# Performance work log

Measured on AMD Instinct MI355X. Metric: run time of the kernel, lower is better.

The kernel has to match this reference:

```python
import jax, jax.numpy as jnp
import numpy as np

N_GRAPHS = 32
N_NODES = 2048          # nodes per graph == lstm1 input_size
N_TOTAL = N_GRAPHS * N_NODES
N_EDGES = 1048576
HEADS = 8
GAT_OUT = 12            # per-head GAT output dim (== num_features)
OUT_CH = 9
NEG_SLOPE = 0.2
BN_EPS = 1e-5


def setup_inputs() -> dict:
    key = jax.random.key(0)
    ks = jax.random.split(key, 20)
    inp = {}
    inp['x'] = jax.random.normal(ks[0], (N_TOTAL, GAT_OUT), jnp.float32)
    inp['edge_index'] = jax.random.randint(ks[1], (2, N_EDGES), 0, N_TOTAL, jnp.int64)
    inp['W_gat'] = jax.random.normal(ks[2], (GAT_OUT, HEADS * GAT_OUT), jnp.float32) * 0.3
    inp['a_src'] = jax.random.normal(ks[3], (HEADS, GAT_OUT), jnp.float32) * 0.3
    inp['a_dst'] = jax.random.normal(ks[4], (HEADS, GAT_OUT), jnp.float32) * 0.3
    inp['gat_bias'] = jax.random.normal(ks[5], (GAT_OUT,), jnp.float32) * 0.1
    inp['bn_gamma'] = jax.random.uniform(ks[6], (GAT_OUT,), jnp.float32, 0.5, 1.5)
    inp['bn_beta'] = jax.random.normal(ks[7], (GAT_OUT,), jnp.float32) * 0.1
    inp['bn_mean'] = jax.random.normal(ks[8], (GAT_OUT,), jnp.float32) * 0.1
    inp['bn_var'] = jax.random.uniform(ks[9], (GAT_OUT,), jnp.float32, 0.5, 1.5)
    inp['w_ih1'] = jax.random.normal(ks[10], (4 * 32, N_NODES), jnp.float32) / np.sqrt(N_NODES)
    inp['w_hh1'] = jax.random.normal(ks[11], (4 * 32, 32), jnp.float32) / np.sqrt(32)
    inp['b_ih1'] = jnp.zeros((4 * 32,), jnp.float32)
    inp['b_hh1'] = jnp.zeros((4 * 32,), jnp.float32)
    inp['w_ih2'] = jax.random.normal(ks[12], (4 * 128, 32), jnp.float32) / np.sqrt(32)
    inp['w_hh2'] = jax.random.normal(ks[13], (4 * 128, 128), jnp.float32) / np.sqrt(128)
    inp['b_ih2'] = jnp.zeros((4 * 128,), jnp.float32)
    inp['b_hh2'] = jnp.zeros((4 * 128,), jnp.float32)
    inp['lin_w'] = jax.random.normal(ks[14], (N_NODES, 128), jnp.float32) / np.sqrt(128)
    inp['lin_b'] = jax.random.normal(ks[15], (N_NODES,), jnp.float32) * 0.1
    return inp


def _gat(x, edge_index, W, a_src, a_dst, bias):
    # PyG GATConv, heads=HEADS, out=GAT_OUT, concat=False (mean over heads), eval mode.
    N = x.shape[0]
    xp = (x @ W).reshape(N, HEADS, GAT_OUT)               # [N,H,C]
    loops = jnp.arange(N, dtype=edge_index.dtype)
    src = jnp.concatenate([edge_index[0], loops])
    dst = jnp.concatenate([edge_index[1], loops])
    asrc = jnp.einsum('nhc,hc->nh', xp, a_src)            # [N,H]
    adst = jnp.einsum('nhc,hc->nh', xp, a_dst)
    e = jax.nn.leaky_relu(asrc[src] + adst[dst], NEG_SLOPE)  # [E,H]
    m = jax.ops.segment_max(e, dst, num_segments=N)
    e = jnp.exp(e - m[dst])
    denom = jax.ops.segment_sum(e, dst, num_segments=N)
    alpha = e / (denom[dst] + 1e-16)
    msg = xp[src] * alpha[:, :, None]                     # [E,H,C]
    out = jax.ops.segment_sum(msg, dst, num_segments=N)   # [N,H,C]
    return out.mean(axis=1) + bias                        # concat=False -> head mean


def _lstm(x_seq, w_ih, w_hh, b_ih, b_hh):
    # x_seq: [T,B,I]; PyTorch gate order i,f,g,o.
    Hh = w_hh.shape[1]
    B = x_seq.shape[1]
    bias = b_ih + b_hh

    def step(carry, xt):
        h, c = carry
        gates = xt @ w_ih.T + h @ w_hh.T + bias
        i, f, g, o = jnp.split(gates, 4, axis=-1)
        c = jax.nn.sigmoid(f) * c + jax.nn.sigmoid(i) * jnp.tanh(g)
        h = jax.nn.sigmoid(o) * jnp.tanh(c)
        return (h, c), h

    init = (jnp.zeros((B, Hh), x_seq.dtype), jnp.zeros((B, Hh), x_seq.dtype))
    _, hs = jax.lax.scan(step, init, x_seq)
    return hs


def reference(x, edge_index, W_gat, a_src, a_dst, gat_bias,
              bn_gamma, bn_beta, bn_mean, bn_var,
              w_ih1, w_hh1, b_ih1, b_hh1,
              w_ih2, w_hh2, b_ih2, b_hh2,
              lin_w, lin_b):
    h = _gat(x, edge_index, W_gat, a_src, a_dst, gat_bias)          # [N,12]
    h = (h - bn_mean) / jnp.sqrt(bn_var + BN_EPS) * bn_gamma + bn_beta
    # dropout inactive in eval mode
    h = jax.nn.log_softmax(h, axis=1)
    h = h.reshape(N_GRAPHS, N_NODES, GAT_OUT)
    h = jnp.moveaxis(h, 2, 0)                                       # [T=12,B,n]
    h = _lstm(h, w_ih1, w_hh1, b_ih1, b_hh1)                        # [12,B,32]
    h = _lstm(h, w_ih2, w_hh2, b_ih2, b_hh2)                        # [12,B,128]
    h = h @ lin_w.T + lin_b                                         # [12,B,n]
    h = h[-OUT_CH:]                                                 # [9,B,n]
    h = jnp.moveaxis(h, 0, 2)                                       # [B,n,9]
    return h.reshape(N_GRAPHS * N_NODES, OUT_CH)
```

## Files before the change

kernel.cpp:

```cpp
#include <hip/hip_runtime.h>
#include <math.h>

#define N_EDGES_C 1048576
#define N_TOTAL_C 65536

typedef _Float16 h2v __attribute__((ext_vector_type(2)));
typedef int i4v __attribute__((ext_vector_type(4)));

#if defined(__has_builtin)
#if __has_builtin(__builtin_amdgcn_fdot2)
#define HAS_FDOT2 1
#endif
#if __has_builtin(__builtin_amdgcn_rcpf)
#define HAS_RCPF 1
#endif
#endif

__device__ __forceinline__ float fdot2(h2v a, h2v b, float c) {
#ifdef HAS_FDOT2
    return __builtin_amdgcn_fdot2(a, b, c, false);
#else
    return c + (float)a.x * (float)b.x + (float)a.y * (float)b.y;
#endif
}

__device__ __forceinline__ float fast_rcp(float x) {
#ifdef HAS_RCPF
    return __builtin_amdgcn_rcpf(x);
#else
    return 1.0f / x;
#endif
}
__device__ __forceinline__ float sigf(float x){ return fast_rcp(1.0f + __expf(-x)); }
__device__ __forceinline__ float tanh_fast(float x){ return fmaf(2.0f, fast_rcp(1.0f + __expf(-2.0f*x)), -1.0f); }
__device__ __forceinline__ float lrelu(float x){ return (x>=0.f)? x : 0.2f*x; }


__global__ void prep_kernel(const float* __restrict__ x, const float* __restrict__ Wg,
                            const float* __restrict__ a_src, const float* __restrict__ a_dst,
                            _Float16* __restrict__ xpp)
{
    int tid = threadIdx.x;
    __shared__ float Ws[12*96];
    __shared__ float as_s[96], ad_s[96];
    for (int i = tid; i < 1152; i += 256) Ws[i] = Wg[i];
    if (tid < 96) { as_s[tid] = a_src[tid]; ad_s[tid] = a_dst[tid]; }
    __syncthreads();
    int gid = blockIdx.x * 256 + tid;
    int n = gid >> 3;
    int h = gid & 7;
    const float4* xv = (const float4*)(x + (size_t)n * 12);
    float4 v0 = xv[0], v1 = xv[1], v2 = xv[2];
    float xr[12] = {v0.x,v0.y,v0.z,v0.w, v1.x,v1.y,v1.z,v1.w, v2.x,v2.y,v2.z,v2.w};
    float xp_[12];
    #pragma unroll
    for (int c = 0; c < 12; c++) {
        float acc = 0.f;
        #pragma unroll
        for (int k = 0; k < 12; k++) acc += xr[k] * Ws[k*96 + h*12 + c];
        xp_[c] = acc;
    }
    float sa = 0.f, sd = 0.f;
    #pragma unroll
    for (int c = 0; c < 12; c++) { sa += xp_[c]*as_s[h*12+c]; sd += xp_[c]*ad_s[h*12+c]; }
    union { _Float16 hh[16]; float ff[8]; float4 f4[2]; } s;
    #pragma unroll
    for (int c = 0; c < 12; c++) s.hh[c] = (_Float16)xp_[c];
    s.ff[6] = sa;
    s.ff[7] = sd;
    float4* o = (float4*)(xpp + (size_t)gid * 16);
    o[0] = s.f4[0];
    o[1] = s.f4[1];
}

__global__ __launch_bounds__(256)
void edge_hist(const int* __restrict__ ei, unsigned* __restrict__ cnt,
               unsigned* __restrict__ rank8)
{
    __shared__ unsigned hist[16384];
    int tid = threadIdx.x;
    int slice = blockIdx.x;
    for (int i = tid; i < 16384; i += 256) hist[i] = 0;
    __syncthreads();
    const i4v* dst4 = (const i4v*)(ei + N_EDGES_C) + slice*2048;
    for (int i = tid; i < 2048; i += 256) {
        i4v d = __builtin_nontemporal_load(&dst4[i]);
        int dd[4] = {d.x, d.y, d.z, d.w};
        unsigned packed = 0;
        #pragma unroll
        for (int j = 0; j < 4; j++) {
            int dj = dd[j];
            unsigned sh = (unsigned)(dj & 3) << 3;
            unsigned old = atomicAdd(&hist[dj >> 2], 1u << sh);
            packed |= ((old >> sh) & 0xffu) << (j*8);
        }
        __builtin_nontemporal_store(packed, &rank8[slice*2048 + i]);
    }
    __syncthreads();
    unsigned* cg = cnt + (size_t)slice*16384;
    for (int i = tid; i < 16384; i += 256) cg[i] = hist[i];
}

__global__ void slice_prefix(unsigned* __restrict__ cnt, int* __restrict__ deg)
{
    int w = blockIdx.x*128 + threadIdx.x;
    unsigned run = 0;
    unsigned* base = cnt + w;
    for (int s = 0; s < 128; s++) {
        unsigned v = base[(size_t)s*16384];
        base[(size_t)s*16384] = run;
        run += v;
    }
    ((int4*)deg)[w] = make_int4((int)(run & 255u), (int)((run >> 8) & 255u),
                                (int)((run >> 16) & 255u), (int)(run >> 24));
}

__global__ void scan_build(const int* __restrict__ deg, int* __restrict__ rowptr)
{
    __shared__ int sums[1024];
    int tid = threadIdx.x;
    int4 v[16];
    const int4* deg4 = (const int4*)deg;
    #pragma unroll
    for (int j = 0; j < 16; j++) v[j] = deg4[tid*16 + j];
    int s = 0;
    #pragma unroll
    for (int j = 0; j < 16; j++) s += v[j].x + v[j].y + v[j].z + v[j].w;
    sums[tid] = s;
    __syncthreads();
    for (int off = 1; off < 1024; off <<= 1) {
        int t = 0;
        if (tid >= off) t = sums[tid - off];
        __syncthreads();
        if (tid >= off) sums[tid] += t;
        __syncthreads();
    }
    int run = sums[tid] - s;
    int4* rp4 = (int4*)rowptr;
    #pragma unroll
    for (int j = 0; j < 16; j++) {
        int4 r;
        r.x = run; run += v[j].x;
        r.y = run; run += v[j].y;
        r.z = run; run += v[j].z;
        r.w = run; run += v[j].w;
        rp4[tid*16 + j] = r;
    }
    if (tid == 1023) rowptr[65536] = run;
}

__global__ __launch_bounds__(256)
void edge_scatter(const int* __restrict__ ei, const unsigned* __restrict__ rank8,
                  const unsigned* __restrict__ cnt, const int* __restrict__ rowptr,
                  int* __restrict__ csr)
{
    __shared__ unsigned pos_s[2048];
    __shared__ int src_s[2048];
    int slice = blockIdx.x >> 2;
    int quar  = blockIdx.x & 3;
    int base = slice*2048 + quar*512;
    const i4v* dst4 = (const i4v*)(ei + N_EDGES_C);
    const i4v* src4 = (const i4v*)ei;
    const unsigned* cslice = cnt + (size_t)slice*16384;
    for (int i = threadIdx.x; i < 512; i += 256) {
        int idx = base + i;
        i4v d = __builtin_nontemporal_load(&dst4[idx]);
        i4v s = __builtin_nontemporal_load(&src4[idx]);
        unsigned r = __builtin_nontemporal_load(&rank8[idx]);
        int dd[4] = {d.x, d.y, d.z, d.w};
        int ss[4] = {s.x, s.y, s.z, s.w};
        #pragma unroll
        for (int j = 0; j < 4; j++) {
            int dj = dd[j];
            unsigned word = cslice[dj >> 2];
            int so = (int)((word >> ((unsigned)(dj & 3) << 3)) & 0xffu);
            int rk = (int)((r >> (j*8)) & 0xffu);
            unsigned pos = (unsigned)(rowptr[dj] + so + rk);
            pos_s[i*4 + j] = pos | ((unsigned)(dj >> 13) << 24);
            src_s[i*4 + j] = ss[j];
        }
    }
    __syncthreads();
    #pragma unroll 1
    for (unsigned g = 0; g < 8; g++) {
        for (int e = threadIdx.x; e < 2048; e += 256) {
            unsigned pw = pos_s[e];
            if ((pw >> 24) == g) csr[pw & 0xFFFFFFu] = src_s[e];
        }
    }
}

__global__ void gat_aggregate(const _Float16* __restrict__ xpp,
                              const int* __restrict__ rowptr, const int* __restrict__ csr_src,
                              const float* __restrict__ gat_bias, const float* __restrict__ bn_gamma,
                              const float* __restrict__ bn_beta, const float* __restrict__ bn_mean,
                              const float* __restrict__ bn_var, float* __restrict__ seq)
{
    int gid = blockIdx.x * 256 + threadIdx.x;
    int n = gid >> 3;
    int h = gid & 7;

    float acc[12];
    float adst_n, d;
    {
        const float4* p = (const float4*)(xpp + (size_t)n*128 + h*16);
        float4 f0 = p[0], f1 = p[1];
        adst_n = f1.w;
        float w = __expf(lrelu(f1.z + adst_n));
        d = w;
        h2v c0 = __builtin_bit_cast(h2v, f0.x), c1 = __builtin_bit_cast(h2v, f0.y);
        h2v c2 = __builtin_bit_cast(h2v, f0.z), c3 = __builtin_bit_cast(h2v, f0.w);
        h2v c4 = __builtin_bit_cast(h2v, f1.x), c5 = __builtin_bit_cast(h2v, f1.y);
        acc[0]=w*(float)c0.x; acc[1]=w*(float)c0.y; acc[2]=w*(float)c1.x; acc[3]=w*(float)c1.y;
        acc[4]=w*(float)c2.x; acc[5]=w*(float)c2.y; acc[6]=w*(float)c3.x; acc[7]=w*(float)c3.y;
        acc[8]=w*(float)c4.x; acc[9]=w*(float)c4.y; acc[10]=w*(float)c5.x; acc[11]=w*(float)c5.y;
    }

    auto accum = [&](float4 f0, float4 f1) {
        float w = __expf(lrelu(f1.z + adst_n));
        d += w;
        h2v c0 = __builtin_bit_cast(h2v, f0.x), c1 = __builtin_bit_cast(h2v, f0.y);
        h2v c2 = __builtin_bit_cast(h2v, f0.z), c3 = __builtin_bit_cast(h2v, f0.w);
        h2v c4 = __builtin_bit_cast(h2v, f1.x), c5 = __builtin_bit_cast(h2v, f1.y);
        acc[0]+=w*(float)c0.x; acc[1]+=w*(float)c0.y; acc[2]+=w*(float)c1.x; acc[3]+=w*(float)c1.y;
        acc[4]+=w*(float)c2.x; acc[5]+=w*(float)c2.y; acc[6]+=w*(float)c3.x; acc[7]+=w*(float)c3.y;
        acc[8]+=w*(float)c4.x; acc[9]+=w*(float)c4.y; acc[10]+=w*(float)c5.x; acc[11]+=w*(float)c5.y;
    };

    int beg = rowptr[n], end = rowptr[n+1];
    const _Float16* xh = xpp + (size_t)h * 16;
    int i = beg;
    for (; i + 4 <= end; i += 4) {
        int s0 = csr_src[i+0];
        int s1 = csr_src[i+1];
        int s2 = csr_src[i+2];
        int s3 = csr_src[i+3];
        const float4* p0 = (const float4*)(xh + (size_t)s0*128);
        const float4* p1 = (const float4*)(xh + (size_t)s1*128);
        const float4* p2 = (const float4*)(xh + (size_t)s2*128);
        const float4* p3 = (const float4*)(xh + (size_t)s3*128);
        float4 a0 = p0[0], b0 = p0[1];
        float4 a1 = p1[0], b1 = p1[1];
        float4 a2 = p2[0], b2 = p2[1];
        float4 a3 = p3[0], b3 = p3[1];
        accum(a0, b0);
        accum(a1, b1);
        accum(a2, b2);
        accum(a3, b3);
    }
    for (; i < end; i++) {
        int src = csr_src[i];
        const float4* p = (const float4*)(xh + (size_t)src*128);
        float4 f0 = p[0], f1 = p[1];
        accum(f0, f1);
    }

    float inv = 1.0f / (d + 1e-16f);
    float res[12];
    #pragma unroll
    for (int c = 0; c < 12; c++) {
        float v = acc[c] * inv;
        v += __shfl_xor(v, 1);
        v += __shfl_xor(v, 2);
        v += __shfl_xor(v, 4);
        res[c] = v * 0.125f;
    }
    if (h == 0) {
        float vals[12];
        float mx = -1e30f;
        #pragma unroll
        for (int c = 0; c < 12; c++) {
            float v = res[c] + gat_bias[c];
            v = (v - bn_mean[c]) * rsqrtf(bn_var[c] + 1e-5f) * bn_gamma[c] + bn_beta[c];
            vals[c] = v;
            mx = fmaxf(mx, v);
        }
        float sum = 0.f;
        #pragma unroll
        for (int c = 0; c < 12; c++) sum += __expf(vals[c] - mx);
        float lse = __logf(sum) + mx;
        #pragma unroll
        for (int c = 0; c < 12; c++) seq[(size_t)c * N_TOTAL_C + n] = vals[c] - lse;
    }
}

__global__ void gemm_x1(const float* __restrict__ A, const float* __restrict__ B,
                        float* __restrict__ C)
{
    __shared__ float As[32][33], Bs[32][33];
    const int K = 2048, N = 128;
    int tid = threadIdx.x;
    int tx = tid & 31, ty = tid >> 5;
    int bm = blockIdx.x * 32, bn = blockIdx.y * 32;
    int kbase = blockIdx.z * 128;
    float acc[4] = {0.f,0.f,0.f,0.f};
    for (int kk = 0; kk < 128; kk += 32) {
        int k0 = kbase + kk;
        #pragma unroll
        for (int i = 0; i < 4; i++) {
            int r = ty + i*8;
            As[r][tx] = A[(size_t)(bm + r) * K + k0 + tx];
            Bs[r][tx] = B[(size_t)(bn + r) * K + k0 + tx];
        }
        __syncthreads();
        #pragma unroll
        for (int k = 0; k < 32; k++) {
            float bv = Bs[tx][k];
            #pragma unroll
            for (int i = 0; i < 4; i++) acc[i] += As[ty + i*8][k] * bv;
        }
        __syncthreads();
    }
    #pragma unroll
    for (int i = 0; i < 4; i++)
        atomicAdd(&C[(size_t)(bm + ty + i*8) * N + bn + tx], acc[i]);
}

__global__ __launch_bounds__(512)
void lstm_fused(const float* __restrict__ X1, const float* __restrict__ w_hh1,
                const float* __restrict__ b_ih1, const float* __restrict__ b_hh1,
                const float* __restrict__ w_ih2, const float* __restrict__ w_hh2,
                const float* __restrict__ b_ih2, const float* __restrict__ b_hh2,
                float* __restrict__ H2)
{
    __shared__ float whh1[128*33];
    __shared__ float b1s[128];
    __shared__ float h1[32], c1[32];
    __shared__ __align__(16) _Float16 h1s[32];
    __shared__ __align__(16) _Float16 h2s[128];
    __shared__ float c2[128];
    __shared__ float g1s[128], g2s[512];
    int tid = threadIdx.x;
    int b = blockIdx.x;

    h2v whh[64];
    {
        const float2* wh = (const float2*)(w_hh2 + (size_t)tid * 128);
        #pragma unroll
        for (int k = 0; k < 64; k++) {
            float2 v = wh[k];
            h2v t; t.x = (_Float16)v.x; t.y = (_Float16)v.y;
            whh[k] = t;
        }
    }
    h2v wih[16];
    {
        const float2* wi = (const float2*)(w_ih2 + (size_t)tid * 32);
        #pragma unroll
        for (int k = 0; k < 16; k++) {
            float2 v = wi[k];
            h2v t; t.x = (_Float16)v.x; t.y = (_Float16)v.y;
            wih[k] = t;
        }
    }
    float b2 = b_ih2[tid] + b_hh2[tid];

    for (int i = tid; i < 128*32; i += 512) whh1[(i >> 5)*33 + (i & 31)] = w_hh1[i];
    if (tid < 128) b1s[tid] = b_ih1[tid] + b_hh1[tid];
    if (tid < 32)  { h1[tid] = 0.f; c1[tid] = 0.f; h1s[tid] = (_Float16)0.f; }
    if (tid < 128) { c2[tid] = 0.f; h2s[tid] = (_Float16)0.f; }

    float xv = 0.f;
    if (tid < 128) xv = X1[((size_t)0*32 + b)*128 + tid];
    __syncthreads();

    for (int t = 0; t < 12; t++) {
        float xv_next = 0.f;
        if (t < 11 && tid < 128) xv_next = X1[((size_t)(t+1)*32 + b)*128 + tid];

        float p0 = b2, p1 = 0.f, p2 = 0.f, p3 = 0.f;
        #pragma unroll
        for (int j = 0; j < 16; j++) {
            float4 f = ((const float4*)h2s)[j];
            p0 = fdot2(__builtin_bit_cast(h2v, f.x), whh[j*4+0], p0);
            p1 = fdot2(__builtin_bit_cast(h2v, f.y), whh[j*4+1], p1);
            p2 = fdot2(__builtin_bit_cast(h2v, f.z), whh[j*4+2], p2);
            p3 = fdot2(__builtin_bit_cast(h2v, f.w), whh[j*4+3], p3);
        }
        float acc2 = (p0 + p1) + (p2 + p3);

        if (tid < 128) {
            const float* wr = &whh1[tid * 33];
            float acc = xv + b1s[tid];
            #pragma unroll
            for (int k = 0; k < 32; k++) acc += h1[k] * wr[k];
            g1s[tid] = acc;
        }
        __syncthreads();
        if (tid < 32) {
            float ig = sigf(g1s[tid]), fg = sigf(g1s[32+tid]);
            float gg = tanh_fast(g1s[64+tid]), og = sigf(g1s[96+tid]);
            float cn = fg * c1[tid] + ig * gg;
            c1[tid] = cn;
            float hn = og * tanh_fast(cn);
            h1[tid] = hn;
            h1s[tid] = (_Float16)hn;
        }
        __syncthreads();
        {
            float q0 = 0.f, q1 = 0.f, q2 = 0.f, q3 = 0.f;
            #pragma unroll
            for (int j = 0; j < 4; j++) {
                float4 f = ((const float4*)h1s)[j];
                q0 = fdot2(__builtin_bit_cast(h2v, f.x), wih[j*4+0], q0);
                q1 = fdot2(__builtin_bit_cast(h2v, f.y), wih[j*4+1], q1);
                q2 = fdot2(__builtin_bit_cast(h2v, f.z), wih[j*4+2], q2);
                q3 = fdot2(__builtin_bit_cast(h2v, f.w), wih[j*4+3], q3);
            }
            g2s[tid] = acc2 + (q0 + q1) + (q2 + q3);
        }
        __syncthreads();
        if (tid < 128) {
            float ig = sigf(g2s[tid]), fg = sigf(g2s[128+tid]);
            float gg = tanh_fast(g2s[256+tid]), og = sigf(g2s[384+tid]);
            float cn = fg * c2[tid] + ig * gg;
            c2[tid] = cn;
            float hn = og * tanh_fast(cn);
            h2s[tid] = (_Float16)hn;
            if (t >= 3) H2[((size_t)t*32 + b)*128 + tid] = hn;
        }
        __syncthreads();
        xv = xv_next;
    }
}

__global__ void gemm_out(const float* __restrict__ A, const float* __restrict__ B,
                         const float* __restrict__ bias, float* __restrict__ out)
{
    __shared__ float As[32][33], Bs[32][33];
    const int K = 128;
    int tid = threadIdx.x;
    int tx = tid & 31, ty = tid >> 5;
    int bm = blockIdx.x * 32, bn = blockIdx.y * 32;
    float acc[4] = {0.f,0.f,0.f,0.f};
    for (int k0 = 0; k0 < K; k0 += 32) {
        #pragma unroll
        for (int i = 0; i < 4; i++) {
            int r = ty + i*8;
            As[r][tx] = A[(size_t)(bm + r) * K + k0 + tx];
            Bs[r][tx] = B[(size_t)(bn + r) * K + k0 + tx];
        }
        __syncthreads();
        #pragma unroll
        for (int kk = 0; kk < 32; kk++) {
            float bv = Bs[tx][kk];
            #pragma unroll
            for (int i = 0; i < 4; i++) acc[i] += As[ty + i*8][kk] * bv;
        }
        __syncthreads();
    }
    int j = blockIdx.x;
    int nn = bn + tx;
    float bv = bias[nn];
    #pragma unroll
    for (int i = 0; i < 4; i++) {
        int bb = ty + i*8;
        out[((size_t)bb * 2048 + nn) * 9 + j] = acc[i] + bv;
    }
}

extern "C" void kernel_launch(void* const* d_in, const int* in_sizes, int n_in,
                              void* d_out, int out_size, void* d_ws, size_t ws_size,
                              hipStream_t stream)
{
    const float* x        = (const float*)d_in[0];
    const int*   ei       = (const int*)  d_in[1];
    const float* W_gat    = (const float*)d_in[2];
    const float* a_src    = (const float*)d_in[3];
    const float* a_dst    = (const float*)d_in[4];
    const float* gat_bias = (const float*)d_in[5];
    const float* bn_gamma = (const float*)d_in[6];
    const float* bn_beta  = (const float*)d_in[7];
    const float* bn_mean  = (const float*)d_in[8];
    const float* bn_var   = (const float*)d_in[9];
    const float* w_ih1    = (const float*)d_in[10];
    const float* w_hh1    = (const float*)d_in[11];
    const float* b_ih1    = (const float*)d_in[12];
    const float* b_hh1    = (const float*)d_in[13];
    const float* w_ih2    = (const float*)d_in[14];
    const float* w_hh2    = (const float*)d_in[15];
    const float* b_ih2    = (const float*)d_in[16];
    const float* b_hh2    = (const float*)d_in[17];
    const float* lin_w    = (const float*)d_in[18];
    const float* lin_b    = (const float*)d_in[19];
    float* out = (float*)d_out;

    float* ws = (float*)d_ws;
    _Float16* xpp = (_Float16*)ws;
    float* seq  = ws + 4194304;
    float* X1   = seq + 786432;
    float* H2   = X1  + 49152;
    int* rowptr = (int*)(H2 + 49152);
    int* deg    = rowptr + 65544;
    unsigned* cnt = (unsigned*)(deg + 65536);
    unsigned* rank8 = cnt + 2097152;
    int* csr    = (int*)(rank8 + 262144);

    hipMemsetAsync(X1, 0, 49152 * sizeof(float), stream);
    prep_kernel <<<2048, 256, 0, stream>>>(x, W_gat, a_src, a_dst, xpp);
    edge_hist   <<<128, 256, 0, stream>>>(ei, cnt, rank8);
    slice_prefix<<<128, 128, 0, stream>>>(cnt, deg);
    scan_build  <<<1, 1024, 0, stream>>>(deg, rowptr);
    edge_scatter<<<512, 256, 0, stream>>>(ei, rank8, cnt, rowptr, csr);
    gat_aggregate<<<2048, 256, 0, stream>>>(xpp, rowptr, csr,
                                            gat_bias, bn_gamma, bn_beta, bn_mean, bn_var, seq);
    gemm_x1<<<dim3(12, 4, 16), 256, 0, stream>>>(seq, w_ih1, X1);
    lstm_fused<<<32, 512, 0, stream>>>(X1, w_hh1, b_ih1, b_hh1, w_ih2, w_hh2, b_ih2, b_hh2, H2);
    gemm_out<<<dim3(9, 64), 256, 0, stream>>>(H2 + 96*128, lin_w, lin_b, out);
}
```

Before: 254.5 us.

## Store projected features head-major and split GAT aggregation per head with reduce kernel

The projected node features are now stored head-major (one contiguous 65536-node plane per head), and the aggregation kernel assigns a whole block to a single head, so each per-edge gather reads 32 bytes from a 2 MB per-head plane instead of a strided slice of a node-major array. The intent is better cache locality for the random source gathers. Per-head results go to a partial buffer, and a new reduce kernel averages the heads and applies bias, batch norm and log-softmax, which costs an extra launch and extra global traffic. The slice_prefix loop is also batched into 32 loads before the stores to raise memory-level parallelism.

```diff
diff --git a/kernel.cpp b/kernel.cpp
--- a/kernel.cpp
+++ b/kernel.cpp
@@ -46,9 +46,8 @@
     for (int i = tid; i < 1152; i += 256) Ws[i] = Wg[i];
     if (tid < 96) { as_s[tid] = a_src[tid]; ad_s[tid] = a_dst[tid]; }
     __syncthreads();
-    int gid = blockIdx.x * 256 + tid;
-    int n = gid >> 3;
-    int h = gid & 7;
+    int h = tid >> 5;
+    int n = blockIdx.x * 32 + (tid & 31);
     const float4* xv = (const float4*)(x + (size_t)n * 12);
     float4 v0 = xv[0], v1 = xv[1], v2 = xv[2];
     float xr[12] = {v0.x,v0.y,v0.z,v0.w, v1.x,v1.y,v1.z,v1.w, v2.x,v2.y,v2.z,v2.w};
@@ -68,7 +67,7 @@
     for (int c = 0; c < 12; c++) s.hh[c] = (_Float16)xp_[c];
     s.ff[6] = sa;
     s.ff[7] = sd;
-    float4* o = (float4*)(xpp + (size_t)gid * 16);
+    float4* o = (float4*)(xpp + ((size_t)h * 65536 + n) * 16);
     o[0] = s.f4[0];
     o[1] = s.f4[1];
 }
@@ -101,15 +100,22 @@
     for (int i = tid; i < 16384; i += 256) cg[i] = hist[i];
 }
 
-__global__ void slice_prefix(unsigned* __restrict__ cnt, int* __restrict__ deg)
+__global__ __launch_bounds__(128)
+void slice_prefix(unsigned* __restrict__ cnt, int* __restrict__ deg)
 {
     int w = blockIdx.x*128 + threadIdx.x;
     unsigned run = 0;
     unsigned* base = cnt + w;
-    for (int s = 0; s < 128; s++) {
-        unsigned v = base[(size_t)s*16384];
-        base[(size_t)s*16384] = run;
-        run += v;
+    #pragma unroll 1
+    for (int s = 0; s < 128; s += 32) {
+        unsigned v[32];
+        #pragma unroll
+        for (int k = 0; k < 32; k++) v[k] = base[(size_t)(s+k)*16384];
+        #pragma unroll
+        for (int k = 0; k < 32; k++) {
+            base[(size_t)(s+k)*16384] = run;
+            run += v[k];
+        }
     }
     ((int4*)deg)[w] = make_int4((int)(run & 255u), (int)((run >> 8) & 255u),
                                 (int)((run >> 16) & 255u), (int)(run >> 24));
@@ -190,20 +196,19 @@
     }
 }
 
-__global__ void gat_aggregate(const _Float16* __restrict__ xpp,
-                              const int* __restrict__ rowptr, const int* __restrict__ csr_src,
-                              const float* __restrict__ gat_bias, const float* __restrict__ bn_gamma,
-                              const float* __restrict__ bn_beta, const float* __restrict__ bn_mean,
-                              const float* __restrict__ bn_var, float* __restrict__ seq)
-{
-    int gid = blockIdx.x * 256 + threadIdx.x;
-    int n = gid >> 3;
-    int h = gid & 7;
+__global__ __launch_bounds__(256)
+void gat_aggregate(const _Float16* __restrict__ xpp,
+                   const int* __restrict__ rowptr, const int* __restrict__ csr_src,
+                   float* __restrict__ partial)
+{
+    int head = blockIdx.x & 7;
+    int n = (blockIdx.x >> 3) * 256 + threadIdx.x;
+    const _Float16* xh = xpp + (size_t)head * (65536 * 16);
 
     float acc[12];
     float adst_n, d;
     {
-        const float4* p = (const float4*)(xpp + (size_t)n*128 + h*16);
+        const float4* p = (const float4*)(xh + (size_t)n * 16);
         float4 f0 = p[0], f1 = p[1];
         adst_n = f1.w;
         float w = __expf(lrelu(f1.z + adst_n));
@@ -228,17 +233,16 @@
     };
 
     int beg = rowptr[n], end = rowptr[n+1];
-    const _Float16* xh = xpp + (size_t)h * 16;
     int i = beg;
     for (; i + 4 <= end; i += 4) {
         int s0 = csr_src[i+0];
         int s1 = csr_src[i+1];
         int s2 = csr_src[i+2];
         int s3 = csr_src[i+3];
-        const float4* p0 = (const float4*)(xh + (size_t)s0*128);
-        const float4* p1 = (const float4*)(xh + (size_t)s1*128);
-        const float4* p2 = (const float4*)(xh + (size_t)s2*128);
-        const float4* p3 = (const float4*)(xh + (size_t)s3*128);
+        const float4* p0 = (const float4*)(xh + (size_t)s0*16);
+        const float4* p1 = (const float4*)(xh + (size_t)s1*16);
+        const float4* p2 = (const float4*)(xh + (size_t)s2*16);
+        const float4* p3 = (const float4*)(xh + (size_t)s3*16);
         float4 a0 = p0[0], b0 = p0[1];
         float4 a1 = p1[0], b1 = p1[1];
         float4 a2 = p2[0], b2 = p2[1];
@@ -250,38 +254,52 @@
     }
     for (; i < end; i++) {
         int src = csr_src[i];
-        const float4* p = (const float4*)(xh + (size_t)src*128);
+        const float4* p = (const float4*)(xh + (size_t)src*16);
         float4 f0 = p[0], f1 = p[1];
         accum(f0, f1);
     }
 
     float inv = 1.0f / (d + 1e-16f);
-    float res[12];
+    #pragma unroll
+    for (int c = 0; c < 12; c++)
+        __builtin_nontemporal_store(acc[c] * inv,
+                                    &partial[((size_t)c*8 + head)*65536 + n]);
+}
+
+__global__ __launch_bounds__(256)
+void gat_reduce(const float* __restrict__ partial,
+                const float* __restrict__ gat_bias, const float* __restrict__ bn_gamma,
+                const float* __restrict__ bn_beta, const float* __restrict__ bn_mean,
+                const float* __restrict__ bn_var, float* __restrict__ seq)
+{
+    int n = blockIdx.x * 256 + threadIdx.x;
+    float vals[12];
+    float mx = -1e30f;
     #pragma unroll
     for (int c = 0; c < 12; c++) {
-        float v = acc[c] * inv;
-        v += __shfl_xor(v, 1);
-        v += __shfl_xor(v, 2);
-        v += __shfl_xor(v, 4);
-        res[c] = v * 0.125f;
-    }
-    if (h == 0) {
-        float vals[12];
-        float mx = -1e30f;
-        #pragma unroll
-        for (int c = 0; c < 12; c++) {
-            float v = res[c] + gat_bias[c];
-            v = (v - bn_mean[c]) * rsqrtf(bn_var[c] + 1e-5f) * bn_gamma[c] + bn_beta[c];
-            vals[c] = v;
-            mx = fmaxf(mx, v);
-        }
-        float sum = 0.f;
-        #pragma unroll
-        for (int c = 0; c < 12; c++) sum += __expf(vals[c] - mx);
-        float lse = __logf(sum) + mx;
-        #pragma unroll
-        for (int c = 0; c < 12; c++) seq[(size_t)c * N_TOTAL_C + n] = vals[c] - lse;
-    }
+        const float* b = partial + (size_t)c*8*65536 + n;
+        float p0 = __builtin_nontemporal_load(b + 0*65536);
+        float p1 = __builtin_nontemporal_load(b + 1*65536);
+        float p2 = __builtin_nontemporal_load(b + 2*65536);
+        float p3 = __builtin_nontemporal_load(b + 3*65536);
+        float p4 = __builtin_nontemporal_load(b + 4*65536);
+        float p5 = __builtin_nontemporal_load(b + 5*65536);
+        float p6 = __builtin_nontemporal_load(b + 6*65536);
+        float p7 = __builtin_nontemporal_load(b + 7*65536);
+        float v = ((p0 + p1) + (p2 + p3)) + ((p4 + p5) + (p6 + p7));
+        float res = v * 0.125f;
+        float t = res + gat_bias[c];
+        t = (t - bn_mean[c]) * rsqrtf(bn_var[c] + 1e-5f) * bn_gamma[c] + bn_beta[c];
+        vals[c] = t;
+        mx = fmaxf(mx, t);
+    }
+    float sum = 0.f;
+    #pragma unroll
+    for (int c = 0; c < 12; c++) sum += __expf(vals[c] - mx);
+    float lse = __logf(sum) + mx;
+    #pragma unroll
+    for (int c = 0; c < 12; c++)
+        __builtin_nontemporal_store(vals[c] - lse, &seq[(size_t)c * N_TOTAL_C + n]);
 }
 
 __global__ void gemm_x1(const float* __restrict__ A, const float* __restrict__ B,
@@ -495,6 +513,7 @@
     unsigned* cnt = (unsigned*)(deg + 65536);
     unsigned* rank8 = cnt + 2097152;
     int* csr    = (int*)(rank8 + 262144);
+    float* partial = (float*)(csr + 1048576);
 
     hipMemsetAsync(X1, 0, 49152 * sizeof(float), stream);
     prep_kernel <<<2048, 256, 0, stream>>>(x, W_gat, a_src, a_dst, xpp);
@@ -502,8 +521,9 @@
     slice_prefix<<<128, 128, 0, stream>>>(cnt, deg);
     scan_build  <<<1, 1024, 0, stream>>>(deg, rowptr);
     edge_scatter<<<512, 256, 0, stream>>>(ei, rank8, cnt, rowptr, csr);
-    gat_aggregate<<<2048, 256, 0, stream>>>(xpp, rowptr, csr,
-                                            gat_bias, bn_gamma, bn_beta, bn_mean, bn_var, seq);
+    gat_aggregate<<<2048, 256, 0, stream>>>(xpp, rowptr, csr, partial);
+    gat_reduce  <<<256, 256, 0, stream>>>(partial, gat_bias, bn_gamma, bn_beta,
+                                          bn_mean, bn_var, seq);
     gemm_x1<<<dim3(12, 4, 16), 256, 0, stream>>>(seq, w_ih1, X1);
     lstm_fused<<<32, 512, 0, stream>>>(X1, w_hh1, b_ih1, b_hh1, w_ih2, w_hh2, b_ih2, b_hh2, H2);
     gemm_out<<<dim3(9, 64), 256, 0, stream>>>(H2 + 96*128, lin_w, lin_b, out);
```

Result: slower. 296.6 us (+16.5%).

## Replace single-block rowptr scan with three-phase parallel block scan

Applied to the files above, without the earlier changes.

The slice_prefix kernel now also does a block-local exclusive scan of node degrees and writes partial rowptr values plus per-block sums. A small scan_mid kernel scans the 128 block sums, and scan_out adds the offsets back, replacing the single 1024-thread scan_build kernel. The per-slice column prefix loop is also batched into 32 loads before the stores to expose memory-level parallelism. This adds one kernel launch and an extra read-modify-write pass over rowptr.

```diff
diff --git a/kernel.cpp b/kernel.cpp
--- a/kernel.cpp
+++ b/kernel.cpp
@@ -101,52 +101,73 @@
     for (int i = tid; i < 16384; i += 256) cg[i] = hist[i];
 }
 
-__global__ void slice_prefix(unsigned* __restrict__ cnt, int* __restrict__ deg)
-{
-    int w = blockIdx.x*128 + threadIdx.x;
+__global__ __launch_bounds__(128)
+void slice_prefix(unsigned* __restrict__ cnt, int* __restrict__ rowptr,
+                  int* __restrict__ chunksum)
+{
+    __shared__ int ss[128];
+    int tid = threadIdx.x;
+    int w = blockIdx.x*128 + tid;
     unsigned run = 0;
     unsigned* base = cnt + w;
-    for (int s = 0; s < 128; s++) {
-        unsigned v = base[(size_t)s*16384];
-        base[(size_t)s*16384] = run;
-        run += v;
-    }
-    ((int4*)deg)[w] = make_int4((int)(run & 255u), (int)((run >> 8) & 255u),
-                                (int)((run >> 16) & 255u), (int)(run >> 24));
-}
-
-__global__ void scan_build(const int* __restrict__ deg, int* __restrict__ rowptr)
-{
-    __shared__ int sums[1024];
-    int tid = threadIdx.x;
-    int4 v[16];
-    const int4* deg4 = (const int4*)deg;
-    #pragma unroll
-    for (int j = 0; j < 16; j++) v[j] = deg4[tid*16 + j];
-    int s = 0;
-    #pragma unroll
-    for (int j = 0; j < 16; j++) s += v[j].x + v[j].y + v[j].z + v[j].w;
-    sums[tid] = s;
-    __syncthreads();
-    for (int off = 1; off < 1024; off <<= 1) {
-        int t = 0;
-        if (tid >= off) t = sums[tid - off];
-        __syncthreads();
-        if (tid >= off) sums[tid] += t;
-        __syncthreads();
-    }
-    int run = sums[tid] - s;
-    int4* rp4 = (int4*)rowptr;
-    #pragma unroll
-    for (int j = 0; j < 16; j++) {
-        int4 r;
-        r.x = run; run += v[j].x;
-        r.y = run; run += v[j].y;
-        r.z = run; run += v[j].z;
-        r.w = run; run += v[j].w;
-        rp4[tid*16 + j] = r;
-    }
-    if (tid == 1023) rowptr[65536] = run;
+    #pragma unroll 1
+    for (int s = 0; s < 128; s += 32) {
+        unsigned v[32];
+        #pragma unroll
+        for (int k = 0; k < 32; k++) v[k] = base[(size_t)(s+k)*16384];
+        #pragma unroll
+        for (int k = 0; k < 32; k++) {
+            base[(size_t)(s+k)*16384] = run;
+            run += v[k];
+        }
+    }
+    int d0 = (int)(run & 255u), d1 = (int)((run >> 8) & 255u);
+    int d2 = (int)((run >> 16) & 255u), d3 = (int)(run >> 24);
+    int tsum = d0 + d1 + d2 + d3;
+    ss[tid] = tsum;
+    __syncthreads();
+    for (int off = 1; off < 128; off <<= 1) {
+        int t = (tid >= off) ? ss[tid - off] : 0;
+        __syncthreads();
+        ss[tid] += t;
+        __syncthreads();
+    }
+    int ex = ss[tid] - tsum;
+    int4 r;
+    r.x = ex;
+    r.y = ex + d0;
+    r.z = ex + d0 + d1;
+    r.w = ex + d0 + d1 + d2;
+    ((int4*)rowptr)[w] = r;
+    if (tid == 127) chunksum[blockIdx.x] = ss[127];
+}
+
+__global__ void scan_mid(const int* __restrict__ chunksum, int* __restrict__ chunkoff,
+                         int* __restrict__ rowptr)
+{
+    __shared__ int ss[128];
+    int tid = threadIdx.x;
+    int v = chunksum[tid];
+    ss[tid] = v;
+    __syncthreads();
+    for (int off = 1; off < 128; off <<= 1) {
+        int t = (tid >= off) ? ss[tid - off] : 0;
+        __syncthreads();
+        ss[tid] += t;
+        __syncthreads();
+    }
+    chunkoff[tid] = ss[tid] - v;
+    if (tid == 127) rowptr[65536] = ss[127];
+}
+
+__global__ __launch_bounds__(128)
+void scan_out(const int* __restrict__ chunkoff, int* __restrict__ rowptr)
+{
+    int w = blockIdx.x*128 + threadIdx.x;
+    int off = chunkoff[blockIdx.x];
+    int4 r = ((int4*)rowptr)[w];
+    r.x += off; r.y += off; r.z += off; r.w += off;
+    ((int4*)rowptr)[w] = r;
 }
 
 __global__ __launch_bounds__(256)
@@ -496,11 +517,15 @@
     unsigned* rank8 = cnt + 2097152;
     int* csr    = (int*)(rank8 + 262144);
 
+    int* chunksum = deg;
+    int* chunkoff = deg + 128;
+
     hipMemsetAsync(X1, 0, 49152 * sizeof(float), stream);
     prep_kernel <<<2048, 256, 0, stream>>>(x, W_gat, a_src, a_dst, xpp);
     edge_hist   <<<128, 256, 0, stream>>>(ei, cnt, rank8);
-    slice_prefix<<<128, 128, 0, stream>>>(cnt, deg);
-    scan_build  <<<1, 1024, 0, stream>>>(deg, rowptr);
+    slice_prefix<<<128, 128, 0, stream>>>(cnt, rowptr, chunksum);
+    scan_mid    <<<1, 128, 0, stream>>>(chunksum, chunkoff, rowptr);
+    scan_out    <<<128, 128, 0, stream>>>(chunkoff, rowptr);
     edge_scatter<<<512, 256, 0, stream>>>(ei, rank8, cnt, rowptr, csr);
     gat_aggregate<<<2048, 256, 0, stream>>>(xpp, rowptr, csr,
                                             gat_bias, bn_gamma, bn_beta, bn_mean, bn_var, seq);
```

After: 243.9 us. -4.1%, faster.
